# Optimization experiments

Measured on AMD Instinct MI355X. Metric: run time of the kernel, lower is better.

Reference implementation:

```python
import jax, jax.numpy as jnp
import numpy as np

KS = 3
ST = 1


def _windows(x, ks, st):
    """im2col sliding windows: (bs, c, h, w) -> (bs, c, H', W', ks, ks)
    where windows[b,c,i,j,k,f] = x[b,c, i*st+k, j*st+f] (matches torch as_strided)."""
    bs, c, h, w = x.shape
    Hp = (h - ks) // st + 1
    Wp = (w - ks) // st + 1
    return jnp.stack(
        [jnp.stack([x[:, :, k:k + Hp * st:st, f:f + Wp * st:st] for f in range(ks)], axis=-1)
         for k in range(ks)], axis=-2)


def setup_inputs() -> dict:
    key = jax.random.key(0)
    k1, k2, k3 = jax.random.split(key, 3)
    x = jax.random.normal(k1, (16, 16, 64, 512), dtype=jnp.float32)
    points = jax.random.normal(k2, (16, 3, 64, 512), dtype=jnp.float32)
    kernel = jax.random.normal(k3, (32, 16, 4), dtype=jnp.float32) * 0.05
    return {"x": x, "kernel": kernel, "points": points}


def reference(x, kernel, points):
    ks, st = KS, ST
    # (bs, in_c, H', W', ks, ks) overlapping patches of features and xyz coords
    strided_x = _windows(x, ks, st)
    strided_pts = _windows(points, ks, st)
    bd = ks // 2 if st == 1 else ks // 4
    # center point of each window: (bs, 3, H', W')
    ctr = points[:, :, bd:-bd, bd:-bd][:, :, ::st, ::st]
    # point-relative coordinates per window element: (bs, 3, H', W', ks, ks)
    rel_pts = ctr[..., None, None] - strided_pts
    # homogeneous coordinate -> d = 4
    rel_pts = jnp.concatenate([rel_pts, jnp.ones_like(rel_pts[:, :1])], axis=1)
    # kernel: (out_c, in_c, 4)
    return jnp.einsum('bdhwkf,bihwkf,oid->bohw', rel_pts, strided_x, kernel)
```

## Files before the change

### kernel.cpp

```cpp
#include <hip/hip_runtime.h>
#include <hip/hip_bf16.h>


#define HH 64
#define WW 512
#define HP 62
#define WP 510
#define IC 16
#define OC 32
#define BS 16
#define RB 2
#define TR (RB + 2)
#define TC 64
#define LC 68
#define NPL 19
#define CPR 17
#define NROWS (NPL * TR)
#define NCHUNK (NROWS * CPR)

typedef __attribute__((ext_vector_type(8))) short short8;
typedef __attribute__((ext_vector_type(4))) float f32x4;

static __device__ __forceinline__ short f2bf(float f) {
    union { __hip_bfloat16 h; short s; } u;
    u.h = __float2bfloat16(f);
    return u.s;
}

__global__ __launch_bounds__(256) void flex_conv_v4(
    const float* __restrict__ x, const float* __restrict__ kern,
    const float* __restrict__ pts, float* __restrict__ out)
{
    __shared__ float lds[NPL * TR * LC];

    const int tid = threadIdx.x;
    const int j0 = blockIdx.x * TC;
    const int i0 = blockIdx.y * RB;
    const int b = blockIdx.z;

    const float* xb = x + (size_t)b * IC * HH * WW;
    const float* pb = pts + (size_t)b * 3 * HH * WW;

    #pragma unroll
    for (int rnd = 0; rnd < 6; ++rnd) {
        const int cid = tid + rnd * 256;
        if (cid < NCHUNK) {
            const int row = cid / CPR;
            const int chunk = cid - row * CPR;
            const int plane = row / TR;
            const int rr = row - plane * TR;
            const float* base = (plane < IC)
                ? (xb + (size_t)plane * HH * WW)
                : (pb + (size_t)(plane - IC) * HH * WW);
            int gcol = j0 + chunk * 4;
            if (gcol > WW - 4) gcol = WW - 4;
            const float* src = base + (size_t)(i0 + rr) * WW + gcol;
            __builtin_amdgcn_global_load_lds(
                (const __attribute__((address_space(1))) void*)src,
                (__attribute__((address_space(3))) void*)(&lds[row * LC + chunk * 4]),
                16, 0, 0);
        }
    }

    const int lane = tid & 63;
    const int wave = tid >> 6;
    const int p = lane & 15;
    const int c = lane >> 4;
    const int tc = wave * 16 + p;

    short8 a0lo, a0hi, a1lo, a1hi;
    {
        const float4* k0v = (const float4*)(kern + (size_t)p * 64 + c * 8);
        const float4* k1v = (const float4*)(kern + (size_t)(16 + p) * 64 + c * 8);
        float4 v0a = k0v[0], v0b = k0v[1], v0c = k0v[8], v0d = k0v[9];
        float4 v1a = k1v[0], v1b = k1v[1], v1c = k1v[8], v1d = k1v[9];
        a0lo[0]=f2bf(v0a.x); a0lo[1]=f2bf(v0a.y); a0lo[2]=f2bf(v0a.z); a0lo[3]=f2bf(v0a.w);
        a0lo[4]=f2bf(v0b.x); a0lo[5]=f2bf(v0b.y); a0lo[6]=f2bf(v0b.z); a0lo[7]=f2bf(v0b.w);
        a0hi[0]=f2bf(v0c.x); a0hi[1]=f2bf(v0c.y); a0hi[2]=f2bf(v0c.z); a0hi[3]=f2bf(v0c.w);
        a0hi[4]=f2bf(v0d.x); a0hi[5]=f2bf(v0d.y); a0hi[6]=f2bf(v0d.z); a0hi[7]=f2bf(v0d.w);
        a1lo[0]=f2bf(v1a.x); a1lo[1]=f2bf(v1a.y); a1lo[2]=f2bf(v1a.z); a1lo[3]=f2bf(v1a.w);
        a1lo[4]=f2bf(v1b.x); a1lo[5]=f2bf(v1b.y); a1lo[6]=f2bf(v1b.z); a1lo[7]=f2bf(v1b.w);
        a1hi[0]=f2bf(v1c.x); a1hi[1]=f2bf(v1c.y); a1hi[2]=f2bf(v1c.z); a1hi[3]=f2bf(v1c.w);
        a1hi[4]=f2bf(v1d.x); a1hi[5]=f2bf(v1d.y); a1hi[6]=f2bf(v1d.z); a1hi[7]=f2bf(v1d.w);
    }

    __syncthreads();

    float xs[4][RB], px0[4][RB], px1[4][RB], px2[4][RB];
    #pragma unroll
    for (int t = 0; t < 4; ++t)
        #pragma unroll
        for (int q = 0; q < RB; ++q) { xs[t][q]=0.f; px0[t][q]=0.f; px1[t][q]=0.f; px2[t][q]=0.f; }
    float c0[RB], c1[RB], c2[RB];

    #pragma unroll
    for (int rr = 0; rr < TR; ++rr) {
        const float* lp0 = &lds[(IC * TR + rr) * LC + tc];
        const float* lp1 = &lds[((IC + 1) * TR + rr) * LC + tc];
        const float* lp2 = &lds[((IC + 2) * TR + rr) * LC + tc];
        const float pa0 = lp0[0], pm0 = lp0[1], pz0 = lp0[2];
        const float pa1 = lp1[0], pm1 = lp1[1], pz1 = lp1[2];
        const float pa2 = lp2[0], pm2 = lp2[1], pz2 = lp2[2];
        if (rr >= 1 && rr <= RB) { c0[rr-1] = pm0; c1[rr-1] = pm1; c2[rr-1] = pm2; }
        #pragma unroll
        for (int t = 0; t < 4; ++t) {
            const int ic = (t >> 1) * 8 + 2 * c + (t & 1);
            const float* lx = &lds[(ic * TR + rr) * LC + tc];
            const float x0 = lx[0], x1 = lx[1], x2 = lx[2];
            const float rsx = x0 + x1 + x2;
            float r0 = pa0 * x0; r0 = fmaf(pm0, x1, r0); r0 = fmaf(pz0, x2, r0);
            float r1 = pa1 * x0; r1 = fmaf(pm1, x1, r1); r1 = fmaf(pz1, x2, r1);
            float r2 = pa2 * x0; r2 = fmaf(pm2, x1, r2); r2 = fmaf(pz2, x2, r2);
            #pragma unroll
            for (int q = 0; q < RB; ++q) {
                if (rr >= q && rr <= q + 2) {
                    xs[t][q] += rsx; px0[t][q] += r0; px1[t][q] += r1; px2[t][q] += r2;
                }
            }
        }
    }

    const int j = j0 + tc;
    #pragma unroll
    for (int q = 0; q < RB; ++q) {
        short8 blo, bhi;
        #pragma unroll
        for (int t = 0; t < 4; ++t) {
            const short t0 = f2bf(fmaf(c0[q], xs[t][q], -px0[t][q]));
            const short t1 = f2bf(fmaf(c1[q], xs[t][q], -px1[t][q]));
            const short t2 = f2bf(fmaf(c2[q], xs[t][q], -px2[t][q]));
            const short t3 = f2bf(xs[t][q]);
            const int s = (t & 1) * 4;
            if (t < 2) { blo[s+0]=t0; blo[s+1]=t1; blo[s+2]=t2; blo[s+3]=t3; }
            else       { bhi[s+0]=t0; bhi[s+1]=t1; bhi[s+2]=t2; bhi[s+3]=t3; }
        }
        f32x4 acc0 = {0.f,0.f,0.f,0.f}, acc1 = {0.f,0.f,0.f,0.f};
        acc0 = __builtin_amdgcn_mfma_f32_16x16x32_bf16(a0lo, blo, acc0, 0, 0, 0);
        acc0 = __builtin_amdgcn_mfma_f32_16x16x32_bf16(a0hi, bhi, acc0, 0, 0, 0);
        acc1 = __builtin_amdgcn_mfma_f32_16x16x32_bf16(a1lo, blo, acc1, 0, 0, 0);
        acc1 = __builtin_amdgcn_mfma_f32_16x16x32_bf16(a1hi, bhi, acc1, 0, 0, 0);
        if (j < WP) {
            float* ob = out + (size_t)b * OC * HP * WP + (size_t)(i0 + q) * WP + j;
            #pragma unroll
            for (int r = 0; r < 4; ++r) {
                const int o = c * 4 + r;
                ob[(size_t)o * HP * WP]        = acc0[r];
                ob[(size_t)(o + 16) * HP * WP] = acc1[r];
            }
        }
    }
}

extern "C" void kernel_launch(void* const* d_in, const int* in_sizes, int n_in,
                              void* d_out, int out_size, void* d_ws, size_t ws_size,
                              hipStream_t stream)
{
    const float* x    = (const float*)d_in[0];
    const float* kern = (const float*)d_in[1];
    const float* pts  = (const float*)d_in[2];
    float* out = (float*)d_out;

    dim3 block(256, 1, 1);
    dim3 grid(WW / TC, HP / RB, BS);
    flex_conv_v4<<<grid, block, 0, stream>>>(x, kern, pts, out);
}
```

Measured before the change: 119.1 us.

## Process four row tiles per block with double-buffered LDS prefetch

Each block now handles four consecutive 2-row tiles instead of one. While the current tile is computed, the next tile is staged asynchronously into a second LDS buffer using global_load_lds. The grid shrinks from 31 to 8 row blocks, and the last tile's start row is clamped, so rows 60–61 are computed and written twice. The aim is to overlap global loads with compute and cut per-block launch and prologue cost; in exchange LDS use per block doubles and there are fewer blocks to spread across CUs.

```diff
diff --git a/kernel.cpp b/kernel.cpp
--- a/kernel.cpp
+++ b/kernel.cpp
@@ -17,6 +17,8 @@
 #define CPR 17
 #define NROWS (NPL * TR)
 #define NCHUNK (NROWS * CPR)
+#define TILEF (NPL * TR * LC)
+#define NT 4
 
 typedef __attribute__((ext_vector_type(8))) short short8;
 typedef __attribute__((ext_vector_type(4))) float f32x4;
@@ -27,20 +29,10 @@
     return u.s;
 }
 
-__global__ __launch_bounds__(256) void flex_conv_v4(
-    const float* __restrict__ x, const float* __restrict__ kern,
-    const float* __restrict__ pts, float* __restrict__ out)
+static __device__ __forceinline__ void stage_tile(
+    const float* __restrict__ xb, const float* __restrict__ pb,
+    float* slot, int i0, int j0, int tid)
 {
-    __shared__ float lds[NPL * TR * LC];
-
-    const int tid = threadIdx.x;
-    const int j0 = blockIdx.x * TC;
-    const int i0 = blockIdx.y * RB;
-    const int b = blockIdx.z;
-
-    const float* xb = x + (size_t)b * IC * HH * WW;
-    const float* pb = pts + (size_t)b * 3 * HH * WW;
-
     #pragma unroll
     for (int rnd = 0; rnd < 6; ++rnd) {
         const int cid = tid + rnd * 256;
@@ -57,10 +49,35 @@
             const float* src = base + (size_t)(i0 + rr) * WW + gcol;
             __builtin_amdgcn_global_load_lds(
                 (const __attribute__((address_space(1))) void*)src,
-                (__attribute__((address_space(3))) void*)(&lds[row * LC + chunk * 4]),
+                (__attribute__((address_space(3))) void*)(slot + row * LC + chunk * 4),
                 16, 0, 0);
         }
     }
+}
+
+__global__ __launch_bounds__(256) void flex_conv_v8(
+    const float* __restrict__ x, const float* __restrict__ kern,
+    const float* __restrict__ pts, float* __restrict__ out)
+{
+    __shared__ float lds[2 * TILEF];
+
+    const int tid = threadIdx.x;
+    const int j0 = blockIdx.x * TC;
+    const int ch = blockIdx.y;
+    const int b = blockIdx.z;
+
+    const float* xb = x + (size_t)b * IC * HH * WW;
+    const float* pb = pts + (size_t)b * 3 * HH * WW;
+
+    int i0s[NT];
+    #pragma unroll
+    for (int u = 0; u < NT; ++u) {
+        int i0 = 2 * (4 * ch + u);
+        if (i0 > HP - RB) i0 = HP - RB;
+        i0s[u] = i0;
+    }
+
+    stage_tile(xb, pb, lds, i0s[0], j0, tid);
 
     const int lane = tid & 63;
     const int wave = tid >> 6;
@@ -86,68 +103,81 @@
 
     __syncthreads();
 
-    float xs[4][RB], px0[4][RB], px1[4][RB], px2[4][RB];
-    #pragma unroll
-    for (int t = 0; t < 4; ++t)
-        #pragma unroll
-        for (int q = 0; q < RB; ++q) { xs[t][q]=0.f; px0[t][q]=0.f; px1[t][q]=0.f; px2[t][q]=0.f; }
-    float c0[RB], c1[RB], c2[RB];
+    const int j = j0 + tc;
+    float* const outb = out + (size_t)b * OC * HP * WP + j;
 
     #pragma unroll
-    for (int rr = 0; rr < TR; ++rr) {
-        const float* lp0 = &lds[(IC * TR + rr) * LC + tc];
-        const float* lp1 = &lds[((IC + 1) * TR + rr) * LC + tc];
-        const float* lp2 = &lds[((IC + 2) * TR + rr) * LC + tc];
-        const float pa0 = lp0[0], pm0 = lp0[1], pz0 = lp0[2];
-        const float pa1 = lp1[0], pm1 = lp1[1], pz1 = lp1[2];
-        const float pa2 = lp2[0], pm2 = lp2[1], pz2 = lp2[2];
-        if (rr >= 1 && rr <= RB) { c0[rr-1] = pm0; c1[rr-1] = pm1; c2[rr-1] = pm2; }
+    for (int u = 0; u < NT; ++u) {
+        if (u + 1 < NT)
+            stage_tile(xb, pb, lds + ((u + 1) & 1) * TILEF, i0s[u + 1], j0, tid);
+
+        const float* slot = lds + (u & 1) * TILEF;
+        const int i0 = i0s[u];
+
+        float xs[4][RB], px0[4][RB], px1[4][RB], px2[4][RB];
         #pragma unroll
-        for (int t = 0; t < 4; ++t) {
-            const int ic = (t >> 1) * 8 + 2 * c + (t & 1);
-            const float* lx = &lds[(ic * TR + rr) * LC + tc];
-            const float x0 = lx[0], x1 = lx[1], x2 = lx[2];
-            const float rsx = x0 + x1 + x2;
-            float r0 = pa0 * x0; r0 = fmaf(pm0, x1, r0); r0 = fmaf(pz0, x2, r0);
-            float r1 = pa1 * x0; r1 = fmaf(pm1, x1, r1); r1 = fmaf(pz1, x2, r1);
-            float r2 = pa2 * x0; r2 = fmaf(pm2, x1, r2); r2 = fmaf(pz2, x2, r2);
+        for (int t = 0; t < 4; ++t)
             #pragma unroll
-            for (int q = 0; q < RB; ++q) {
-                if (rr >= q && rr <= q + 2) {
-                    xs[t][q] += rsx; px0[t][q] += r0; px1[t][q] += r1; px2[t][q] += r2;
+            for (int q = 0; q < RB; ++q) { xs[t][q]=0.f; px0[t][q]=0.f; px1[t][q]=0.f; px2[t][q]=0.f; }
+        float c0[RB], c1[RB], c2[RB];
+
+        #pragma unroll
+        for (int rr = 0; rr < TR; ++rr) {
+            const float* lp0 = slot + (IC * TR + rr) * LC + tc;
+            const float* lp1 = slot + ((IC + 1) * TR + rr) * LC + tc;
+            const float* lp2 = slot + ((IC + 2) * TR + rr) * LC + tc;
+            const float pa0 = lp0[0], pm0 = lp0[1], pz0 = lp0[2];
+            const float pa1 = lp1[0], pm1 = lp1[1], pz1 = lp1[2];
+            const float pa2 = lp2[0], pm2 = lp2[1], pz2 = lp2[2];
+            if (rr >= 1 && rr <= RB) { c0[rr-1] = pm0; c1[rr-1] = pm1; c2[rr-1] = pm2; }
+            #pragma unroll
+            for (int t = 0; t < 4; ++t) {
+                const int icp = (t >> 1) * 8 + 2 * c + (t & 1);
+                const float* lx = slot + (icp * TR + rr) * LC + tc;
+                const float x0 = lx[0], x1 = lx[1], x2 = lx[2];
+                const float rsx = x0 + x1 + x2;
+                float r0 = pa0 * x0; r0 = fmaf(pm0, x1, r0); r0 = fmaf(pz0, x2, r0);
+                float r1 = pa1 * x0; r1 = fmaf(pm1, x1, r1); r1 = fmaf(pz1, x2, r1);
+                float r2 = pa2 * x0; r2 = fmaf(pm2, x1, r2); r2 = fmaf(pz2, x2, r2);
+                #pragma unroll
+                for (int q = 0; q < RB; ++q) {
+                    if (rr >= q && rr <= q + 2) {
+                        xs[t][q] += rsx; px0[t][q] += r0; px1[t][q] += r1; px2[t][q] += r2;
+                    }
                 }
             }
         }
-    }
 
-    const int j = j0 + tc;
-    #pragma unroll
-    for (int q = 0; q < RB; ++q) {
-        short8 blo, bhi;
         #pragma unroll
-        for (int t = 0; t < 4; ++t) {
-            const short t0 = f2bf(fmaf(c0[q], xs[t][q], -px0[t][q]));
-            const short t1 = f2bf(fmaf(c1[q], xs[t][q], -px1[t][q]));
-            const short t2 = f2bf(fmaf(c2[q], xs[t][q], -px2[t][q]));
-            const short t3 = f2bf(xs[t][q]);
-            const int s = (t & 1) * 4;
-            if (t < 2) { blo[s+0]=t0; blo[s+1]=t1; blo[s+2]=t2; blo[s+3]=t3; }
-            else       { bhi[s+0]=t0; bhi[s+1]=t1; bhi[s+2]=t2; bhi[s+3]=t3; }
-        }
-        f32x4 acc0 = {0.f,0.f,0.f,0.f}, acc1 = {0.f,0.f,0.f,0.f};
-        acc0 = __builtin_amdgcn_mfma_f32_16x16x32_bf16(a0lo, blo, acc0, 0, 0, 0);
-        acc0 = __builtin_amdgcn_mfma_f32_16x16x32_bf16(a0hi, bhi, acc0, 0, 0, 0);
-        acc1 = __builtin_amdgcn_mfma_f32_16x16x32_bf16(a1lo, blo, acc1, 0, 0, 0);
-        acc1 = __builtin_amdgcn_mfma_f32_16x16x32_bf16(a1hi, bhi, acc1, 0, 0, 0);
-        if (j < WP) {
-            float* ob = out + (size_t)b * OC * HP * WP + (size_t)(i0 + q) * WP + j;
+        for (int q = 0; q < RB; ++q) {
+            short8 blo, bhi;
             #pragma unroll
-            for (int r = 0; r < 4; ++r) {
-                const int o = c * 4 + r;
-                ob[(size_t)o * HP * WP]        = acc0[r];
-                ob[(size_t)(o + 16) * HP * WP] = acc1[r];
+            for (int t = 0; t < 4; ++t) {
+                const short t0 = f2bf(fmaf(c0[q], xs[t][q], -px0[t][q]));
+                const short t1 = f2bf(fmaf(c1[q], xs[t][q], -px1[t][q]));
+                const short t2 = f2bf(fmaf(c2[q], xs[t][q], -px2[t][q]));
+                const short t3 = f2bf(xs[t][q]);
+                const int s = (t & 1) * 4;
+                if (t < 2) { blo[s+0]=t0; blo[s+1]=t1; blo[s+2]=t2; blo[s+3]=t3; }
+                else       { bhi[s+0]=t0; bhi[s+1]=t1; bhi[s+2]=t2; bhi[s+3]=t3; }
+            }
+            f32x4 acc0 = {0.f,0.f,0.f,0.f}, acc1 = {0.f,0.f,0.f,0.f};
+            acc0 = __builtin_amdgcn_mfma_f32_16x16x32_bf16(a0lo, blo, acc0, 0, 0, 0);
+            acc0 = __builtin_amdgcn_mfma_f32_16x16x32_bf16(a0hi, bhi, acc0, 0, 0, 0);
+            acc1 = __builtin_amdgcn_mfma_f32_16x16x32_bf16(a1lo, blo, acc1, 0, 0, 0);
+            acc1 = __builtin_amdgcn_mfma_f32_16x16x32_bf16(a1hi, bhi, acc1, 0, 0, 0);
+            if (j < WP) {
+                float* ob = outb + (size_t)(i0 + q) * WP;
+                #pragma unroll
+                for (int r = 0; r < 4; ++r) {
+                    const int o = c * 4 + r;
+                    ob[(size_t)o * HP * WP]        = acc0[r];
+                    ob[(size_t)(o + 16) * HP * WP] = acc1[r];
+                }
             }
         }
+
+        if (u + 1 < NT) __syncthreads();
     }
 }
 
@@ -161,6 +191,6 @@
     float* out = (float*)d_out;
 
     dim3 block(256, 1, 1);
-    dim3 grid(WW / TC, HP / RB, BS);
-    flex_conv_v4<<<grid, block, 0, stream>>>(x, kern, pts, out);
+    dim3 grid(WW / TC, 8, BS);
+    flex_conv_v8<<<grid, block, 0, stream>>>(x, kern, pts, out);
 }
```

Measured after the change: 117.1 us. No clear change (-1.6%).
